# Optimization experiments

Hardware: AMD Instinct MI355X
Metric: run time of the kernel (lower is better)

The kernel has to match this reference:

```python
import jax, jax.numpy as jnp
import numpy as np

D = 128
N = 768
EPS = 1e-5

def _layernorm(x, w, b):
    m = jnp.mean(x, axis=-1, keepdims=True)
    v = jnp.mean(jnp.square(x - m), axis=-1, keepdims=True)
    return (x - m) * jax.lax.rsqrt(v + EPS) * w + b

def _linear(x, w, b):
    # torch Linear convention: w is [out, in]
    return jnp.einsum('...i,oi->...o', x, w) + b

def setup_inputs() -> dict:
    key = jax.random.key(0)
    ks = jax.random.split(key, 8)
    s = 1.0 / np.sqrt(D)
    d = {
        'pair': jax.random.normal(ks[0], (N, N, D), dtype=jnp.float32),
        'ln_in_w': jnp.ones((D,), jnp.float32), 'ln_in_b': jnp.zeros((D,), jnp.float32),
        'lp_w': jax.random.uniform(ks[1], (D, D), jnp.float32, -s, s), 'lp_b': jnp.zeros((D,), jnp.float32),
        'lg_w': jax.random.uniform(ks[2], (D, D), jnp.float32, -s, s), 'lg_b': jnp.zeros((D,), jnp.float32),
        'rp_w': jax.random.uniform(ks[3], (D, D), jnp.float32, -s, s), 'rp_b': jnp.zeros((D,), jnp.float32),
        'rg_w': jax.random.uniform(ks[4], (D, D), jnp.float32, -s, s), 'rg_b': jnp.zeros((D,), jnp.float32),
        'cn_w': jnp.ones((D,), jnp.float32), 'cn_b': jnp.zeros((D,), jnp.float32),
        'op_w': jax.random.uniform(ks[5], (D, D), jnp.float32, -s, s), 'op_b': jnp.zeros((D,), jnp.float32),
        'og_w': jax.random.uniform(ks[6], (D, D), jnp.float32, -s, s), 'og_b': jnp.zeros((D,), jnp.float32),
        'ln_out_w': jnp.ones((D,), jnp.float32), 'ln_out_b': jnp.zeros((D,), jnp.float32),
    }
    return d

def reference(pair, ln_in_w, ln_in_b, lp_w, lp_b, lg_w, lg_b, rp_w, rp_b, rg_w, rg_b,
              cn_w, cn_b, op_w, op_b, og_w, og_b, ln_out_w, ln_out_b):
    z = _layernorm(pair, ln_in_w, ln_in_b)
    left = jax.nn.sigmoid(_linear(z, lg_w, lg_b)) * _linear(z, lp_w, lp_b)
    right = jax.nn.sigmoid(_linear(z, rg_w, rg_b)) * _linear(z, rp_w, rp_b)
    # outgoing direction: pair(i,j) = sum_k left(i,k,d) * right(j,k,d)
    tri = jnp.einsum('ikd,jkd->ijd', left, right)
    tri = _layernorm(tri, cn_w, cn_b)
    tri = jax.nn.sigmoid(_linear(pair, og_w, og_b)) * _linear(tri, op_w, op_b)
    return _layernorm(pair + tri, ln_out_w, ln_out_b)
```

## Files before the change

### kernel.cpp

```cpp
#include <hip/hip_runtime.h>

#define N 768
#define D 128
#define NSQ (N*N)
#define EPS 1e-5f

typedef __bf16 bf16;
typedef __bf16 bf16x4 __attribute__((ext_vector_type(4)));
typedef __bf16 bf16x8 __attribute__((ext_vector_type(8)));
typedef float f32x4 __attribute__((ext_vector_type(4)));

__device__ __forceinline__ void gld16(const void* g, void* l) {
    __builtin_amdgcn_global_load_lds(
        (const __attribute__((address_space(1))) unsigned int*)g,
        (__attribute__((address_space(3))) unsigned int*)l, 16, 0, 0);
}

__device__ __forceinline__ void barrier_lds() {
    asm volatile("s_waitcnt lgkmcnt(0)" ::: "memory");
    __builtin_amdgcn_s_barrier();
    __builtin_amdgcn_sched_barrier(0);
}

__global__ void k_convert_w(const float* __restrict__ lp, const float* __restrict__ lg,
                            const float* __restrict__ rp, const float* __restrict__ rg,
                            const float* __restrict__ op, const float* __restrict__ og,
                            bf16* __restrict__ dst) {
    const float* srcs[6] = {lp, lg, rp, rg, op, og};
    int m = blockIdx.y;
    int i = blockIdx.x * 256 + threadIdx.x;
    dst[m * 16384 + i] = (bf16)srcs[m][i];
}

__global__ __launch_bounds__(512, 2) void k_ln_gate2(
    const float* __restrict__ pair, const float* __restrict__ lnw, const float* __restrict__ lnb,
    const bf16* __restrict__ wbf,
    const float* __restrict__ lp_b, const float* __restrict__ lg_b,
    const float* __restrict__ rp_b, const float* __restrict__ rg_b,
    bf16* __restrict__ left_t, bf16* __restrict__ right_t)
{
    __shared__ bf16 zt[2][64 * 128];

    const int t = threadIdx.x;
    const int lane = t & 63, wid = t >> 6;
    const int side = wid >> 2, dq = wid & 3;
    const int lr = lane & 15, lh = lane >> 4;

    const bf16* wPsrc = wbf + (side ? 2 : 0) * 16384;
    const bf16* wGsrc = wbf + (side ? 3 : 1) * 16384;
    const float* bPp = side ? rp_b : lp_b;
    const float* bGp = side ? rg_b : lg_b;
    bf16* dst = side ? right_t : left_t;

    bf16x8 aP[4][2], aG[4][2];
    #pragma unroll
    for (int kk = 0; kk < 4; ++kk)
        #pragma unroll
        for (int m = 0; m < 2; ++m) {
            int rd = dq * 32 + m * 16 + lr;
            aP[kk][m] = *(const bf16x8*)(wPsrc + rd * 128 + (kk * 4 + lh) * 8);
            aG[kk][m] = *(const bf16x8*)(wGsrc + rd * 128 + (kk * 4 + lh) * 8);
        }
    float bP[2], bG[2];
    #pragma unroll
    for (int m = 0; m < 2; ++m) {
        bP[m] = bPp[dq * 32 + m * 16 + lr];
        bG[m] = bGp[dq * 32 + m * 16 + lr];
    }

    const int r8 = t >> 3, q = t & 7;

    f32x4 lw0 = *(const f32x4*)(lnw + q * 16);
    f32x4 lw1 = *(const f32x4*)(lnw + q * 16 + 4);
    f32x4 lw2 = *(const f32x4*)(lnw + q * 16 + 8);
    f32x4 lw3 = *(const f32x4*)(lnw + q * 16 + 12);
    f32x4 lb0 = *(const f32x4*)(lnb + q * 16);
    f32x4 lb1 = *(const f32x4*)(lnb + q * 16 + 4);
    f32x4 lb2 = *(const f32x4*)(lnb + q * 16 + 8);
    f32x4 lb3 = *(const f32x4*)(lnb + q * 16 + 12);

    const int bid = blockIdx.x, gstride = gridDim.x;

    f32x4 p0, p1, p2, p3;
    {
        const float* prow = pair + (size_t)(bid * 64 + r8) * 128 + q * 16;
        p0 = *(const f32x4*)(prow);
        p1 = *(const f32x4*)(prow + 4);
        p2 = *(const f32x4*)(prow + 8);
        p3 = *(const f32x4*)(prow + 12);
    }

    int buf = 0;
    for (int tile = bid; tile < NSQ / 64; tile += gstride) {
        const int row0 = tile * 64;

        float x[16];
        #pragma unroll
        for (int e = 0; e < 4; ++e) {
            x[e] = p0[e]; x[4 + e] = p1[e]; x[8 + e] = p2[e]; x[12 + e] = p3[e];
        }
        float s1 = 0.f, s2 = 0.f;
        #pragma unroll
        for (int j = 0; j < 16; ++j) { s1 += x[j]; s2 += x[j] * x[j]; }
        s1 += __shfl_xor(s1, 1); s2 += __shfl_xor(s2, 1);
        s1 += __shfl_xor(s1, 2); s2 += __shfl_xor(s2, 2);
        s1 += __shfl_xor(s1, 4); s2 += __shfl_xor(s2, 4);
        float mean = s1 * (1.f / 128.f);
        float rstd = rsqrtf(s2 * (1.f / 128.f) - mean * mean + EPS);

        bf16x8 pk0, pk1;
        #pragma unroll
        for (int e = 0; e < 4; ++e) {
            pk0[e]     = (bf16)((x[e]      - mean) * rstd * lw0[e] + lb0[e]);
            pk0[4 + e] = (bf16)((x[4 + e]  - mean) * rstd * lw1[e] + lb1[e]);
            pk1[e]     = (bf16)((x[8 + e]  - mean) * rstd * lw2[e] + lb2[e]);
            pk1[4 + e] = (bf16)((x[12 + e] - mean) * rstd * lw3[e] + lb3[e]);
        }
        {
            char* zb = (char*)&zt[buf][0];
            *(bf16x8*)(zb + r8 * 256 + ((q * 2)     ^ (r8 & 7)) * 16) = pk0;
            *(bf16x8*)(zb + r8 * 256 + ((q * 2 + 1) ^ (r8 & 7)) * 16) = pk1;
        }
        barrier_lds();

        int nt = tile + gstride;
        if (nt < NSQ / 64) {
            const float* prow = pair + (size_t)(nt * 64 + r8) * 128 + q * 16;
            p0 = *(const f32x4*)(prow);
            p1 = *(const f32x4*)(prow + 4);
            p2 = *(const f32x4*)(prow + 8);
            p3 = *(const f32x4*)(prow + 12);
        }

        f32x4 accP[2][4] = {};
        f32x4 accG[2][4] = {};
        const char* zb = (const char*)&zt[buf][0];
        #pragma unroll
        for (int kk = 0; kk < 4; ++kk) {
            bf16x8 bz[4];
            #pragma unroll
            for (int n = 0; n < 4; ++n) {
                int rz = n * 16 + lr;
                bz[n] = *(const bf16x8*)(zb + rz * 256 + (((kk * 4 + lh)) ^ (rz & 7)) * 16);
            }
            #pragma unroll
            for (int m = 0; m < 2; ++m)
                #pragma unroll
                for (int n = 0; n < 4; ++n) {
                    accP[m][n] = __builtin_amdgcn_mfma_f32_16x16x32_bf16(bz[n], aP[kk][m], accP[m][n], 0, 0, 0);
                    accG[m][n] = __builtin_amdgcn_mfma_f32_16x16x32_bf16(bz[n], aG[kk][m], accG[m][n], 0, 0, 0);
                }
        }

        #pragma unroll
        for (int m = 0; m < 2; ++m) {
            const int d = dq * 32 + m * 16 + lr;
            bf16* drow = dst + (size_t)d * NSQ + row0 + lh * 4;
            #pragma unroll
            for (int n = 0; n < 4; ++n) {
                bf16x4 pk;
                #pragma unroll
                for (int reg = 0; reg < 4; ++reg) {
                    float g = accG[m][n][reg] + bG[m];
                    float p = accP[m][n][reg] + bP[m];
                    pk[reg] = (bf16)(p * (1.f / (1.f + __expf(-g))));
                }
                *(bf16x4*)(drow + n * 16) = pk;
            }
        }
        buf ^= 1;
    }
}

__global__ __launch_bounds__(512, 2) void k_tri(
    const bf16* __restrict__ left_t, const bf16* __restrict__ right_t, bf16* __restrict__ tri_t)
{
    __shared__ bf16 at[2][256 * 64];
    __shared__ bf16 bt[2][256 * 64];
    const int t = threadIdx.x;
    const int b = blockIdx.x;
    const int xcd = b & 7;
    const int s = b >> 3;
    const int d = xcd * 16 + s / 9;
    const int tile = s % 9;
    const int ti = tile / 3, tj = tile % 3;
    const bf16* A = left_t + (size_t)d * NSQ;
    const bf16* B = right_t + (size_t)d * NSQ;
    const int i0 = ti * 256, j0 = tj * 256;

    auto stage = [&](int buf, int kt) {
        int k0 = kt * 64;
        #pragma unroll
        for (int c = 0; c < 4; ++c) {
            int sl = c * 512 + t;
            int r = sl >> 3, cp = sl & 7, cl = cp ^ (r & 7);
            gld16(A + (size_t)(i0 + r) * 768 + k0 + cl * 8, (char*)at[buf] + sl * 16);
            gld16(B + (size_t)(j0 + r) * 768 + k0 + cl * 8, (char*)bt[buf] + sl * 16);
        }
    };

    const int lane = t & 63, wid = t >> 6;
    const int wr = wid >> 2, wc = wid & 3;
    const int lr = lane & 15, lh = lane >> 4;

    f32x4 acc[8][4] = {};

    stage(0, 0);
    for (int kt = 0; kt < 12; ++kt) {
        asm volatile("s_waitcnt vmcnt(0)" ::: "memory");
        __builtin_amdgcn_s_barrier();
        __builtin_amdgcn_sched_barrier(0);

        const int buf = kt & 1;
        if (kt < 11) stage(buf ^ 1, kt + 1);

        const char* ab = (const char*)at[buf];
        const char* bb = (const char*)bt[buf];
        #pragma unroll
        for (int kk = 0; kk < 2; ++kk) {
            bf16x8 bff[4];
            #pragma unroll
            for (int n = 0; n < 4; ++n) {
                int r = wc * 64 + n * 16 + lr;
                int phys = (kk * 4 + lh) ^ (r & 7);
                bff[n] = *(const bf16x8*)(bb + r * 128 + phys * 16);
            }
            #pragma unroll
            for (int m = 0; m < 8; ++m) {
                int r = wr * 128 + m * 16 + lr;
                int phys = (kk * 4 + lh) ^ (r & 7);
                bf16x8 af = *(const bf16x8*)(ab + r * 128 + phys * 16);
                #pragma unroll
                for (int n = 0; n < 4; ++n)
                    acc[m][n] = __builtin_amdgcn_mfma_f32_16x16x32_bf16(bff[n], af, acc[m][n], 0, 0, 0);
            }
        }
    }

    bf16* C = tri_t + (size_t)d * NSQ;
    #pragma unroll
    for (int m = 0; m < 8; ++m) {
        const int ri = i0 + wr * 128 + m * 16 + lr;
        bf16* crow = C + (size_t)ri * 768 + j0 + wc * 64 + lh * 4;
        #pragma unroll
        for (int n = 0; n < 4; ++n) {
            bf16x4 pk;
            #pragma unroll
            for (int reg = 0; reg < 4; ++reg)
                pk[reg] = (bf16)acc[m][n][reg];
            *(bf16x4*)(crow + n * 16) = pk;
        }
    }
}

__global__ __launch_bounds__(256, 2) void k_cln(
    const bf16* __restrict__ tri_t, const float* __restrict__ cnw, const float* __restrict__ cnb,
    bf16* __restrict__ tri_ln)
{
    __shared__ bf16 tile[256 * 128];
    __shared__ float mrs[256][2];
    const int t = threadIdx.x;
    const size_t ij = (size_t)blockIdx.x * 256 + t;
    float s1 = 0.f, s2 = 0.f;
    for (int dc = 0; dc < 16; ++dc) {
        bf16x8 pk;
        #pragma unroll
        for (int e = 0; e < 8; ++e) {
            int dd = dc * 8 + e;
            bf16 raw = tri_t[(size_t)dd * NSQ + ij];
            float v = (float)raw;
            s1 += v; s2 += v * v;
            pk[e] = raw;
        }
        *(bf16x8*)((char*)tile + t * 256 + (dc ^ (t & 7)) * 16) = pk;
    }
    float mean = s1 * (1.f / 128.f);
    float rstd = rsqrtf(s2 * (1.f / 128.f) - mean * mean + EPS);
    mrs[t][0] = mean; mrs[t][1] = rstd;
    __syncthreads();
    const size_t ij0 = (size_t)blockIdx.x * 256;
    #pragma unroll
    for (int c = 0; c < 16; ++c) {
        int sl = c * 256 + t;
        int rl = sl >> 4, cp = sl & 15, cl = cp ^ (rl & 7);
        bf16x8 raw = *(const bf16x8*)((const char*)tile + rl * 256 + cp * 16);
        float m = mrs[rl][0], r = mrs[rl][1];
        f32x4 w0 = *(const f32x4*)(cnw + cl * 8);
        f32x4 w1 = *(const f32x4*)(cnw + cl * 8 + 4);
        f32x4 b0 = *(const f32x4*)(cnb + cl * 8);
        f32x4 b1 = *(const f32x4*)(cnb + cl * 8 + 4);
        bf16x8 o;
        #pragma unroll
        for (int e = 0; e < 4; ++e) {
            o[e]     = (bf16)(((float)raw[e]     - m) * r * w0[e] + b0[e]);
            o[4 + e] = (bf16)(((float)raw[4 + e] - m) * r * w1[e] + b1[e]);
        }
        *(bf16x8*)(tri_ln + (ij0 + rl) * 128 + cl * 8) = o;
    }
}

__global__ __launch_bounds__(512, 2) void k_final2(
    const float* __restrict__ pair, const bf16* __restrict__ tri_ln,
    const bf16* __restrict__ wbf,
    const float* __restrict__ op_b, const float* __restrict__ og_b,
    const float* __restrict__ lnow, const float* __restrict__ lnob,
    float* __restrict__ out)
{
    __shared__ bf16 zt[64 * 128];
    __shared__ bf16 tt[2][64 * 128];
    __shared__ bf16 ub[64 * 136];

    const int t = threadIdx.x;
    const int lane = t & 63, wid = t >> 6;
    const int dq = wid & 3, wh = wid >> 2;
    const int lr = lane & 15, lh = lane >> 4;

    const bf16* opsrc = wbf + 4 * 16384;
    const bf16* ogsrc = wbf + 5 * 16384;

    bf16x8 aOG[4][2], aOP[4][2];
    #pragma unroll
    for (int kk = 0; kk < 4; ++kk)
        #pragma unroll
        for (int m = 0; m < 2; ++m) {
            int rd = dq * 32 + m * 16 + lr;
            aOG[kk][m] = *(const bf16x8*)(ogsrc + rd * 128 + (kk * 4 + lh) * 8);
            aOP[kk][m] = *(const bf16x8*)(opsrc + rd * 128 + (kk * 4 + lh) * 8);
        }
    f32x4 vbOG[2], vbOP[2];
    #pragma unroll
    for (int m = 0; m < 2; ++m) {
        vbOG[m] = *(const f32x4*)(og_b + dq * 32 + m * 16 + lh * 4);
        vbOP[m] = *(const f32x4*)(op_b + dq * 32 + m * 16 + lh * 4);
    }

    const int r8 = t >> 3, q = t & 7;
    f32x4 lw0 = *(const f32x4*)(lnow + q * 16);
    f32x4 lw1 = *(const f32x4*)(lnow + q * 16 + 4);
    f32x4 lw2 = *(const f32x4*)(lnow + q * 16 + 8);
    f32x4 lw3 = *(const f32x4*)(lnow + q * 16 + 12);
    f32x4 lb0 = *(const f32x4*)(lnob + q * 16);
    f32x4 lb1 = *(const f32x4*)(lnob + q * 16 + 4);
    f32x4 lb2 = *(const f32x4*)(lnob + q * 16 + 8);
    f32x4 lb3 = *(const f32x4*)(lnob + q * 16 + 12);

    const int bid = blockIdx.x, gstride = gridDim.x;

    auto stage_tt = [&](int buf, int tile) {
        const int row0 = tile * 64;
        #pragma unroll
        for (int c = 0; c < 2; ++c) {
            int s = c * 512 + t;
            int r = s >> 4, cp = s & 15, cl = cp ^ (r & 7);
            gld16(tri_ln + (size_t)(row0 + r) * 128 + cl * 8, (char*)tt[buf] + s * 16);
        }
    };

    stage_tt(0, bid);
    f32x4 pA0, pA1, pA2, pA3;
    {
        const float* prow = pair + (size_t)(bid * 64 + r8) * 128 + q * 16;
        pA0 = *(const f32x4*)(prow);
        pA1 = *(const f32x4*)(prow + 4);
        pA2 = *(const f32x4*)(prow + 8);
        pA3 = *(const f32x4*)(prow + 12);
    }

    int buf = 0;
    for (int tile = bid; tile < NSQ / 64; tile += gstride) {
        const int row0 = tile * 64;

        {
            bf16x8 pk0, pk1;
            #pragma unroll
            for (int e = 0; e < 4; ++e) {
                pk0[e]     = (bf16)pA0[e];
                pk0[4 + e] = (bf16)pA1[e];
                pk1[e]     = (bf16)pA2[e];
                pk1[4 + e] = (bf16)pA3[e];
            }
            char* zb = (char*)zt;
            *(bf16x8*)(zb + r8 * 256 + ((q * 2)     ^ (r8 & 7)) * 16) = pk0;
            *(bf16x8*)(zb + r8 * 256 + ((q * 2 + 1) ^ (r8 & 7)) * 16) = pk1;
        }
        barrier_lds();

        const int nt = tile + gstride;
        if (nt < NSQ / 64) stage_tt(buf ^ 1, nt);

        f32x4 pB0 = pA0, pB1 = pA1, pB2 = pA2, pB3 = pA3;
        if (nt < NSQ / 64) {
            const float* prow = pair + (size_t)(nt * 64 + r8) * 128 + q * 16;
            pB0 = *(const f32x4*)(prow);
            pB1 = *(const f32x4*)(prow + 4);
            pB2 = *(const f32x4*)(prow + 8);
            pB3 = *(const f32x4*)(prow + 12);
        }

        f32x4 accOG[2][2] = {};
        f32x4 accOP[2][2] = {};
        const char* zb = (const char*)zt;
        const char* tb = (const char*)tt[buf];
        #pragma unroll
        for (int kk = 0; kk < 4; ++kk) {
            bf16x8 bzp[2], bzt[2];
            #pragma unroll
            for (int n = 0; n < 2; ++n) {
                int rz = wh * 32 + n * 16 + lr;
                int phys = (kk * 4 + lh) ^ (rz & 7);
                bzp[n] = *(const bf16x8*)(zb + rz * 256 + phys * 16);
                bzt[n] = *(const bf16x8*)(tb + rz * 256 + phys * 16);
            }
            #pragma unroll
            for (int m = 0; m < 2; ++m)
                #pragma unroll
                for (int n = 0; n < 2; ++n) {
                    accOG[m][n] = __builtin_amdgcn_mfma_f32_16x16x32_bf16(aOG[kk][m], bzp[n], accOG[m][n], 0, 0, 0);
                    accOP[m][n] = __builtin_amdgcn_mfma_f32_16x16x32_bf16(aOP[kk][m], bzt[n], accOP[m][n], 0, 0, 0);
                }
        }

        #pragma unroll
        for (int m = 0; m < 2; ++m)
            #pragma unroll
            for (int n = 0; n < 2; ++n) {
                int rr = wh * 32 + n * 16 + lr;
                bf16x4 v;
                #pragma unroll
                for (int reg = 0; reg < 4; ++reg) {
                    float g = accOG[m][n][reg] + vbOG[m][reg];
                    float p = accOP[m][n][reg] + vbOP[m][reg];
                    v[reg] = (bf16)(p * (1.f / (1.f + __expf(-g))));
                }
                *(bf16x4*)(ub + rr * 136 + dq * 32 + m * 16 + lh * 4) = v;
            }
        barrier_lds();

        {
            float x[16];
            const bf16* ur = ub + r8 * 136 + q * 16;
            bf16x8 u0 = *(const bf16x8*)(ur);
            bf16x8 u1 = *(const bf16x8*)(ur + 8);
            #pragma unroll
            for (int e = 0; e < 4; ++e) {
                x[e]      = pA0[e] + (float)u0[e];
                x[4 + e]  = pA1[e] + (float)u0[4 + e];
                x[8 + e]  = pA2[e] + (float)u1[e];
                x[12 + e] = pA3[e] + (float)u1[4 + e];
            }
            float s1 = 0.f, s2 = 0.f;
            #pragma unroll
            for (int j = 0; j < 16; ++j) { s1 += x[j]; s2 += x[j] * x[j]; }
            s1 += __shfl_xor(s1, 1); s2 += __shfl_xor(s2, 1);
            s1 += __shfl_xor(s1, 2); s2 += __shfl_xor(s2, 2);
            s1 += __shfl_xor(s1, 4); s2 += __shfl_xor(s2, 4);
            float mean = s1 * (1.f / 128.f);
            float rstd = rsqrtf(s2 * (1.f / 128.f) - mean * mean + EPS);
            float* orow = out + (size_t)(row0 + r8) * 128 + q * 16;
            f32x4 o0, o1, o2, o3;
            #pragma unroll
            for (int e = 0; e < 4; ++e) {
                o0[e] = (x[e]      - mean) * rstd * lw0[e] + lb0[e];
                o1[e] = (x[4 + e]  - mean) * rstd * lw1[e] + lb1[e];
                o2[e] = (x[8 + e]  - mean) * rstd * lw2[e] + lb2[e];
                o3[e] = (x[12 + e] - mean) * rstd * lw3[e] + lb3[e];
            }
            *(f32x4*)(orow)      = o0;
            *(f32x4*)(orow + 4)  = o1;
            *(f32x4*)(orow + 8)  = o2;
            *(f32x4*)(orow + 12) = o3;
        }

        pA0 = pB0; pA1 = pB1; pA2 = pB2; pA3 = pB3;
        buf ^= 1;
    }
}

extern "C" void kernel_launch(void* const* d_in, const int* in_sizes, int n_in,
                              void* d_out, int out_size, void* d_ws, size_t ws_size,
                              hipStream_t stream) {
    const float* pair    = (const float*)d_in[0];
    const float* ln_in_w = (const float*)d_in[1];
    const float* ln_in_b = (const float*)d_in[2];
    const float* lp_w    = (const float*)d_in[3];
    const float* lp_b    = (const float*)d_in[4];
    const float* lg_w    = (const float*)d_in[5];
    const float* lg_b    = (const float*)d_in[6];
    const float* rp_w    = (const float*)d_in[7];
    const float* rp_b    = (const float*)d_in[8];
    const float* rg_w    = (const float*)d_in[9];
    const float* rg_b    = (const float*)d_in[10];
    const float* cn_w    = (const float*)d_in[11];
    const float* cn_b    = (const float*)d_in[12];
    const float* op_w    = (const float*)d_in[13];
    const float* op_b    = (const float*)d_in[14];
    const float* og_w    = (const float*)d_in[15];
    const float* og_b    = (const float*)d_in[16];
    const float* ln_out_w = (const float*)d_in[17];
    const float* ln_out_b = (const float*)d_in[18];

    const size_t HALF = (size_t)128 * NSQ * 2;
    char* ws = (char*)d_ws;
    bf16* wbf     = (bf16*)ws;
    bf16* right_t = (bf16*)(ws + 196608);
    bf16* tri_ln  = right_t;
    bf16* left_t  = (bf16*)d_out;
    bf16* tri_t   = (bf16*)((char*)d_out + HALF);

    k_convert_w<<<dim3(64, 6), 256, 0, stream>>>(lp_w, lg_w, rp_w, rg_w, op_w, og_w, wbf);
    k_ln_gate2<<<dim3(512), 512, 0, stream>>>(pair, ln_in_w, ln_in_b, wbf,
                                              lp_b, lg_b, rp_b, rg_b, left_t, right_t);
    k_tri<<<dim3(1152), 512, 0, stream>>>(left_t, right_t, tri_t);
    k_cln<<<dim3(NSQ / 256), 256, 0, stream>>>(tri_t, cn_w, cn_b, tri_ln);
    k_final2<<<dim3(512), 512, 0, stream>>>(pair, tri_ln, wbf, op_b, og_b,
                                            ln_out_w, ln_out_b, (float*)d_out);
}
```

Baseline: 569.9 us.

## Interleave tri GEMM mainloop into quarter phases with staged loads and setprio

```diff
diff --git a/kernel.cpp b/kernel.cpp
--- a/kernel.cpp
+++ b/kernel.cpp
@@ -188,52 +188,73 @@
     const bf16* B = right_t + (size_t)d * NSQ;
     const int i0 = ti * 256, j0 = tj * 256;
 
-    auto stage = [&](int buf, int kt) {
-        int k0 = kt * 64;
-        #pragma unroll
-        for (int c = 0; c < 4; ++c) {
-            int sl = c * 512 + t;
-            int r = sl >> 3, cp = sl & 7, cl = cp ^ (r & 7);
-            gld16(A + (size_t)(i0 + r) * 768 + k0 + cl * 8, (char*)at[buf] + sl * 16);
-            gld16(B + (size_t)(j0 + r) * 768 + k0 + cl * 8, (char*)bt[buf] + sl * 16);
-        }
-    };
-
     const int lane = t & 63, wid = t >> 6;
     const int wr = wid >> 2, wc = wid & 3;
     const int lr = lane & 15, lh = lane >> 4;
 
+    auto stage_quarter = [&](int bf, int kt, int qq) {
+        const int k0 = kt * 64;
+        #pragma unroll
+        for (int c = 0; c < 2; ++c) {
+            int sl = qq * 1024 + c * 512 + t;
+            int r = sl >> 3, cp = sl & 7, cl = cp ^ (r & 7);
+            gld16(A + (size_t)(i0 + r) * 768 + k0 + cl * 8, (char*)at[bf] + sl * 16);
+            gld16(B + (size_t)(j0 + r) * 768 + k0 + cl * 8, (char*)bt[bf] + sl * 16);
+        }
+    };
+
     f32x4 acc[8][4] = {};
-
-    stage(0, 0);
+    bf16x8 bff[4][2];
+
+    stage_quarter(0, 0, 0);
+    stage_quarter(0, 0, 1);
+    asm volatile("s_waitcnt vmcnt(0)" ::: "memory");
+    __builtin_amdgcn_s_barrier();
+    __builtin_amdgcn_sched_barrier(0);
+
     for (int kt = 0; kt < 12; ++kt) {
-        asm volatile("s_waitcnt vmcnt(0)" ::: "memory");
-        __builtin_amdgcn_s_barrier();
-        __builtin_amdgcn_sched_barrier(0);
-
-        const int buf = kt & 1;
-        if (kt < 11) stage(buf ^ 1, kt + 1);
-
-        const char* ab = (const char*)at[buf];
-        const char* bb = (const char*)bt[buf];
-        #pragma unroll
-        for (int kk = 0; kk < 2; ++kk) {
-            bf16x8 bff[4];
-            #pragma unroll
-            for (int n = 0; n < 4; ++n) {
-                int r = wc * 64 + n * 16 + lr;
-                int phys = (kk * 4 + lh) ^ (r & 7);
-                bff[n] = *(const bf16x8*)(bb + r * 128 + phys * 16);
-            }
-            #pragma unroll
-            for (int m = 0; m < 8; ++m) {
-                int r = wr * 128 + m * 16 + lr;
-                int phys = (kk * 4 + lh) ^ (r & 7);
-                bf16x8 af = *(const bf16x8*)(ab + r * 128 + phys * 16);
+        const int bf = kt & 1;
+        const char* ab = (const char*)at[bf];
+        const char* bb = (const char*)bt[bf];
+        #pragma unroll
+        for (int q = 0; q < 4; ++q) {
+            bf16x8 af[2][2];
+            #pragma unroll
+            for (int m2 = 0; m2 < 2; ++m2)
+                #pragma unroll
+                for (int kk = 0; kk < 2; ++kk) {
+                    int r = wr * 128 + (q * 2 + m2) * 16 + lr;
+                    int phys = (kk * 4 + lh) ^ (r & 7);
+                    af[m2][kk] = *(const bf16x8*)(ab + r * 128 + phys * 16);
+                }
+            if (q == 0) {
                 #pragma unroll
                 for (int n = 0; n < 4; ++n)
-                    acc[m][n] = __builtin_amdgcn_mfma_f32_16x16x32_bf16(bff[n], af, acc[m][n], 0, 0, 0);
-            }
+                    #pragma unroll
+                    for (int kk = 0; kk < 2; ++kk) {
+                        int r = wc * 64 + n * 16 + lr;
+                        int phys = (kk * 4 + lh) ^ (r & 7);
+                        bff[n][kk] = *(const bf16x8*)(bb + r * 128 + phys * 16);
+                    }
+            }
+            if (q < 2 && kt < 11) stage_quarter(bf ^ 1, kt + 1, q);
+
+            __builtin_amdgcn_s_barrier();
+            asm volatile("s_waitcnt lgkmcnt(0)" ::: "memory");
+            __builtin_amdgcn_sched_barrier(0);
+            __builtin_amdgcn_s_setprio(1);
+            #pragma unroll
+            for (int kk = 0; kk < 2; ++kk)
+                #pragma unroll
+                for (int m2 = 0; m2 < 2; ++m2)
+                    #pragma unroll
+                    for (int n = 0; n < 4; ++n)
+                        acc[q * 2 + m2][n] = __builtin_amdgcn_mfma_f32_16x16x32_bf16(
+                            bff[n][kk], af[m2][kk], acc[q * 2 + m2][n], 0, 0, 0);
+            __builtin_amdgcn_s_setprio(0);
+            if (q == 3) asm volatile("s_waitcnt vmcnt(0)" ::: "memory");
+            __builtin_amdgcn_s_barrier();
+            __builtin_amdgcn_sched_barrier(0);
         }
     }
 
```

Measured after the change: 569.0 us. No clear change (-0.1%).
